# Kernel optimization log

Hardware: AMD Instinct MI355X
Metric: run time of the kernel (lower is better)

## Reference

```python
import jax, jax.numpy as jnp
import numpy as np

B, LQ, H, NH, LK, N = 32, 256, 256, 8, 512, 8192
DH = H // NH
EPS = 1e-12

def layer_norm(x, g, b):
    m = x.mean(-1, keepdims=True)
    v = ((x - m) ** 2).mean(-1, keepdims=True)
    return (x - m) / jnp.sqrt(v + EPS) * g + b

def setup_inputs() -> dict:
    rs = np.random.RandomState(0)
    counts = rs.randint(LK // 2, LK + 1, size=B)  # ragged per-graph edge counts, max = LK
    E = int(counts.sum())
    edge_batch = jnp.asarray(np.repeat(np.arange(B), counts), jnp.int32)
    edge_pos = jnp.asarray(np.concatenate([np.arange(c) for c in counts]), jnp.int32)
    pad_mask = jnp.asarray((np.arange(LK)[None, :] < counts[:, None]).astype(np.float32))
    src = jnp.asarray(rs.randint(0, N, E), jnp.int32)
    dst = jnp.asarray(rs.randint(0, N, E), jnp.int32)
    ks = jax.random.split(jax.random.key(0), 16)
    def rn(i, shape, s=0.02):
        return jax.random.normal(ks[i], shape, jnp.float32) * s
    return dict(
        extended_attention_mask=jnp.zeros((B, 1, 1, LQ), jnp.float32),
        query=rn(0, (B, LQ, H), 1.0),
        rel_embedding_output=rn(1, (E, H), 1.0),
        graph_output=rn(2, (N, H), 1.0),
        src=src, dst=dst, edge_batch=edge_batch, edge_pos=edge_pos, pad_mask=pad_mask,
        Wq=rn(3, (H, H)), bq=jnp.zeros((H,), jnp.float32),
        Wk=rn(4, (2 * H, H)), bk=jnp.zeros((H,), jnp.float32),
        Wv=rn(5, (H, H)), bv=jnp.zeros((H,), jnp.float32),
        Wo=rn(6, (H, H)), bo=jnp.zeros((H,), jnp.float32),
        ln1_g=jnp.ones((H,), jnp.float32), ln1_b=jnp.zeros((H,), jnp.float32),
        W1=rn(7, (H, H)), b1=jnp.zeros((H,), jnp.float32),
        W2=rn(8, (H, H)), b2=jnp.zeros((H,), jnp.float32),
        ln2_g=jnp.ones((H,), jnp.float32), ln2_b=jnp.zeros((H,), jnp.float32),
    )

def reference(extended_attention_mask, query, rel_embedding_output, graph_output,
              src, dst, edge_batch, edge_pos, pad_mask,
              Wq, bq, Wk, bk, Wv, bv, Wo, bo, ln1_g, ln1_b,
              W1, b1, W2, b2, ln2_g, ln2_b):
    # --- memory_transform: edge gather + ragged pad (vectorized scatter) ---
    key_flat = jnp.concatenate([graph_output[src], rel_embedding_output], -1)  # [E, 2H]
    dst_flat = graph_output[dst]                                               # [E, H]
    key_pad = jnp.zeros((B, LK, 2 * H), key_flat.dtype).at[edge_batch, edge_pos].set(key_flat)
    val_pad = jnp.zeros((B, LK, H), dst_flat.dtype).at[edge_batch, edge_pos].set(dst_flat)
    cross_mask = (1.0 - pad_mask)[:, None, None, :] * -10000.0                 # [B,1,1,LK]
    # --- BidiAttention ---
    Q = (query @ Wq + bq).reshape(B, LQ, NH, DH)
    K = (key_pad @ Wk + bk).reshape(B, LK, NH, DH)
    V = (val_pad @ Wv + bv).reshape(B, LK, NH, DH)
    scores = jnp.einsum('bqhd,bkhd->bhqk', Q, K) / np.float32(np.sqrt(DH))
    pq = jax.nn.softmax(scores + cross_mask, axis=-1)
    query_ctx = jnp.einsum('bhqk,bkhd->bqhd', pq, V).reshape(B, LQ, H)
    pv = jax.nn.softmax(scores.transpose(0, 1, 3, 2) + extended_attention_mask, axis=-1)
    value_ctx = jnp.einsum('bhkq,bqhd->bkhd', pv, Q).reshape(B, LK, H)
    # --- RelAwareCross output / gate ---
    query_out = layer_norm(query_ctx @ Wo + bo + query, ln1_g, ln1_b)
    theta = jax.nn.sigmoid(value_ctx @ W1 + b1 + val_pad @ W2 + b2)
    value_new = layer_norm(theta * value_ctx + (1.0 - theta) * val_pad, ln2_g, ln2_b)
    # --- memory_update: unpad + scatter-mean by dst, replace rows with incoming edges ---
    val_edges = value_new[edge_batch, edge_pos]                                # [E, H]
    sums = jax.ops.segment_sum(val_edges, dst, num_segments=N)
    cnts = jax.ops.segment_sum(jnp.ones((val_edges.shape[0],), val_edges.dtype), dst, num_segments=N)
    mean = sums / jnp.maximum(cnts, 1.0)[:, None]
    graph_new = jnp.where((cnts > 0)[:, None], mean, graph_output)
    return (graph_new, query_out)
```

## Files before the change

kernel.cpp:

```cpp
#include <hip/hip_runtime.h>
#include <hip/hip_bf16.h>
#include <string.h>

#define B_ 32
#define LQ_ 256
#define H_ 256
#define NH_ 8
#define LK_ 512
#define N_ 8192
#define DH_ 32

typedef float floatx4 __attribute__((ext_vector_type(4)));
typedef short shortx8 __attribute__((ext_vector_type(8)));
typedef short shortx4 __attribute__((ext_vector_type(4)));

__device__ __forceinline__ short f2b(float f) {
    __hip_bfloat16 h = __float2bfloat16(f);
    short s;
    __builtin_memcpy(&s, &h, 2);
    return s;
}
__device__ __forceinline__ float b2f(short s) {
    unsigned u = ((unsigned)(unsigned short)s) << 16;
    float f;
    __builtin_memcpy(&f, &u, 4);
    return f;
}

#define LOG2E 1.44269504088896f

__global__ __launch_bounds__(256) void phase1(
    const float* __restrict__ graph, const float* __restrict__ rel,
    const int* __restrict__ src, const int* __restrict__ dst,
    const int* __restrict__ eb, const int* __restrict__ ep,
    const float* __restrict__ pad_mask,
    const float* __restrict__ Wq, const float* __restrict__ Wk,
    const float* __restrict__ Wv, const float* __restrict__ Wo,
    const float* __restrict__ W1, const float* __restrict__ W2,
    short* __restrict__ WT, short* __restrict__ key_pad,
    short* __restrict__ val_pad, int* __restrict__ head,
    int* __restrict__ row2e, int E) {
    const int bid = blockIdx.x, tid = threadIdx.x;
    if (bid < 8192) {
        int row = bid * 2 + (tid >> 7);
        int t = tid & 127;
        int b = row >> 9, p = row & 511;
        bool valid = pad_mask[row] > 0.5f;
        size_t krow = (size_t)row * 512;
        size_t vrow = (size_t)row * 256;
        int kc = t * 4, vc = t * 2;
        if (valid) {
            int lo = 0, hi = E;
            while (lo < hi) { int mid = (lo + hi) >> 1; if (eb[mid] < b) lo = mid + 1; else hi = mid; }
            int e = lo + p;
            int s = src[e], d = dst[e];
            const float* sp = (kc < 256) ? (graph + (size_t)s * 256 + kc)
                                         : (rel + (size_t)e * 256 + (kc - 256));
            float4 k4 = *(const float4*)sp;
            key_pad[krow + kc + 0] = f2b(k4.x);
            key_pad[krow + kc + 1] = f2b(k4.y);
            key_pad[krow + kc + 2] = f2b(k4.z);
            key_pad[krow + kc + 3] = f2b(k4.w);
            float2 v2 = *(const float2*)(graph + (size_t)d * 256 + vc);
            val_pad[vrow + vc + 0] = f2b(v2.x);
            val_pad[vrow + vc + 1] = f2b(v2.y);
        } else {
            *(long long*)&key_pad[krow + kc] = 0;
            *(int*)&val_pad[vrow + vc] = 0;
        }
    } else if (bid < 9984) {
        int i = (bid - 8192) * 256 + tid;
        const float* s;
        int K, loc;
        if (i < 65536) { s = Wq; K = 256; loc = i; }
        else if (i < 196608) { s = Wk; K = 512; loc = i - 65536; }
        else {
            int m = (i - 196608) >> 16;
            loc = (i - 196608) & 65535;
            K = 256;
            s = (m == 0) ? Wv : (m == 1) ? Wo : (m == 2) ? W1 : W2;
        }
        int n = loc / K, k = loc - n * K;
        WT[i] = f2b(s[(size_t)k * 256 + n]);
    } else {
        int i = (bid - 9984) * 256 + tid;
        if (i < 8192) head[i] = -1;
        for (int j = i; j < E; j += 8192)
            row2e[eb[j] * 512 + ep[j]] = j;
    }
}

__global__ __launch_bounds__(256) void phase2_gemm(
    const float* __restrict__ query, const short* __restrict__ key_pad,
    const short* __restrict__ val_pad, const short* __restrict__ WT,
    const float* __restrict__ bq, const float* __restrict__ bk,
    const float* __restrict__ bv,
    short* __restrict__ Qb, short* __restrict__ Kb,
    short* __restrict__ Vt, short* __restrict__ Qt) {
    __shared__ short As[64][40];
    __shared__ short Bs[64][40];
    const int tid = threadIdx.x;
    const int id = blockIdx.x;
    const float* Af = nullptr; const short* Ab = nullptr;
    const float* Bf = nullptr; const short* Bb = nullptr;
    const float* bias; short* C;
    size_t cbase; int cstride, K; bool biasM;
    if (id < 512) {
        int rb = id >> 2, cb = id & 3;
        Af = query + (size_t)(rb * 64) * 256; K = 256;
        Bb = WT + (size_t)(cb * 64) * 256;
        bias = bq + cb * 64; biasM = false;
        C = Qb; cbase = (size_t)(rb * 64) * 256 + cb * 64; cstride = 256;
    } else if (id < 1536) {
        int t = id - 512; int rb = t >> 2, cb = t & 3;
        Ab = key_pad + (size_t)(rb * 64) * 512; K = 512;
        Bb = WT + 65536 + (size_t)(cb * 64) * 512;
        bias = bk + cb * 64; biasM = false;
        C = Kb; cbase = (size_t)(rb * 64) * 256 + cb * 64; cstride = 256;
    } else if (id < 2560) {
        int t = id - 1536; int b = t >> 5, ct = (t >> 3) & 3, kt = t & 7;
        Ab = WT + 196608 + (size_t)(ct * 64) * 256; K = 256;
        Bb = val_pad + ((size_t)(b * 512 + kt * 64)) * 256;
        bias = bv + ct * 64; biasM = true;
        C = Vt; cbase = ((size_t)(b * 256 + ct * 64)) * 512 + kt * 64; cstride = 512;
    } else {
        int t = id - 2560; int b = t >> 4, ct = (t >> 2) & 3, qt = t & 3;
        Ab = WT + (size_t)(ct * 64) * 256; K = 256;
        Bf = query + ((size_t)(b * 256 + qt * 64)) * 256;
        bias = bq + ct * 64; biasM = true;
        C = Qt; cbase = ((size_t)(b * 256 + ct * 64)) * 256 + qt * 64; cstride = 256;
    }
    const int wv = tid >> 6, lane = tid & 63;
    const int mw = (wv & 1) * 32, nw = (wv >> 1) * 32;
    const int lm = lane & 15, quad = lane >> 4;

    floatx4 acc[2][2] = {{{0.f, 0.f, 0.f, 0.f}, {0.f, 0.f, 0.f, 0.f}},
                         {{0.f, 0.f, 0.f, 0.f}, {0.f, 0.f, 0.f, 0.f}}};

    for (int kc = 0; kc < K; kc += 32) {
        int r = tid >> 2, kq = (tid & 3) * 8;
        if (Af) {
            const float* ap = Af + (size_t)r * K + kc + kq;
            float4 a1 = *(const float4*)ap, a2 = *(const float4*)(ap + 4);
            As[r][kq + 0] = f2b(a1.x); As[r][kq + 1] = f2b(a1.y);
            As[r][kq + 2] = f2b(a1.z); As[r][kq + 3] = f2b(a1.w);
            As[r][kq + 4] = f2b(a2.x); As[r][kq + 5] = f2b(a2.y);
            As[r][kq + 6] = f2b(a2.z); As[r][kq + 7] = f2b(a2.w);
        } else {
            *(shortx8*)&As[r][kq] = *(const shortx8*)(Ab + (size_t)r * K + kc + kq);
        }
        if (Bf) {
            const float* bp = Bf + (size_t)r * K + kc + kq;
            float4 b1 = *(const float4*)bp, b2 = *(const float4*)(bp + 4);
            Bs[r][kq + 0] = f2b(b1.x); Bs[r][kq + 1] = f2b(b1.y);
            Bs[r][kq + 2] = f2b(b1.z); Bs[r][kq + 3] = f2b(b1.w);
            Bs[r][kq + 4] = f2b(b2.x); Bs[r][kq + 5] = f2b(b2.y);
            Bs[r][kq + 6] = f2b(b2.z); Bs[r][kq + 7] = f2b(b2.w);
        } else {
            *(shortx8*)&Bs[r][kq] = *(const shortx8*)(Bb + (size_t)r * K + kc + kq);
        }
        __syncthreads();
        shortx8 a0 = *(const shortx8*)&As[mw + lm][quad * 8];
        shortx8 a1 = *(const shortx8*)&As[mw + 16 + lm][quad * 8];
        shortx8 b0 = *(const shortx8*)&Bs[nw + lm][quad * 8];
        shortx8 b1 = *(const shortx8*)&Bs[nw + 16 + lm][quad * 8];
        acc[0][0] = __builtin_amdgcn_mfma_f32_16x16x32_bf16(a0, b0, acc[0][0], 0, 0, 0);
        acc[0][1] = __builtin_amdgcn_mfma_f32_16x16x32_bf16(a0, b1, acc[0][1], 0, 0, 0);
        acc[1][0] = __builtin_amdgcn_mfma_f32_16x16x32_bf16(a1, b0, acc[1][0], 0, 0, 0);
        acc[1][1] = __builtin_amdgcn_mfma_f32_16x16x32_bf16(a1, b1, acc[1][1], 0, 0, 0);
        __syncthreads();
    }
#pragma unroll
    for (int i = 0; i < 2; i++) {
#pragma unroll
        for (int j = 0; j < 2; j++) {
            int gn = nw + j * 16 + lm;
#pragma unroll
            for (int r = 0; r < 4; r++) {
                int gm = mw + i * 16 + quad * 4 + r;
                float bvv = biasM ? bias[gm] : bias[gn];
                C[cbase + (size_t)gm * cstride + gn] = f2b(acc[i][j][r] + bvv);
            }
        }
    }
}

__global__ __launch_bounds__(512, 4) void phase3_attn(
    const short* __restrict__ Qm, const short* __restrict__ Km,
    const short* __restrict__ Vt, const short* __restrict__ Qt,
    const float* __restrict__ pad_mask, const float* __restrict__ ext,
    short* __restrict__ qctx, short* __restrict__ vctx) {
    __shared__ short SA[128][40];
    __shared__ short ST[32][136];
    __shared__ short P[8][32][72];
    const int tid = threadIdx.x;
    const int w = tid >> 6, lane = tid & 63;
    const int lm = lane & 15, quad = lane >> 4;
    const float scale2 = 0.17677669529663687f * LOG2E;
    const int id = blockIdx.x;
    short (*Pw)[72] = P[w];

    if (id < 256) {
        const int b = id >> 3, h = id & 7;
        shortx8 bqf[2];
        bqf[0] = *(const shortx8*)(Qm + ((size_t)(b * 256 + w * 32 + lm)) * 256 + h * 32 + quad * 8);
        bqf[1] = *(const shortx8*)(Qm + ((size_t)(b * 256 + w * 32 + 16 + lm)) * 256 + h * 32 + quad * 8);
        floatx4 oacc[2][2] = {{{0.f,0.f,0.f,0.f},{0.f,0.f,0.f,0.f}},
                              {{0.f,0.f,0.f,0.f},{0.f,0.f,0.f,0.f}}};
        float psum[2] = {0.f, 0.f};
        const floatx4* pmp = (const floatx4*)(pad_mask + b * 512);
        for (int kc = 0; kc < 512; kc += 128) {
            if (tid < 256) {
                int r = tid >> 1, dq = (tid & 1) * 16;
                const short* kp = Km + ((size_t)(b * 512 + kc + r)) * 256 + h * 32 + dq;
                *(shortx8*)&SA[r][dq] = *(const shortx8*)kp;
                *(shortx8*)&SA[r][dq + 8] = *(const shortx8*)(kp + 8);
            } else {
                int u = tid - 256;
                int r = u >> 3, kq = (u & 7) * 16;
                const short* vp = Vt + ((size_t)(b * 256 + h * 32 + r)) * 512 + kc + kq;
                *(shortx8*)&ST[r][kq] = *(const shortx8*)vp;
                *(shortx8*)&ST[r][kq + 8] = *(const shortx8*)(vp + 8);
            }
            __syncthreads();
#pragma unroll
            for (int kh = 0; kh < 2; kh++) {
#pragma unroll
                for (int kt = 0; kt < 4; kt++) {
                    shortx8 ak = *(const shortx8*)&SA[kh * 64 + kt * 16 + lm][quad * 8];
                    floatx4 pm = pmp[kc / 4 + kh * 16 + kt * 4 + quad];
#pragma unroll
                    for (int qf = 0; qf < 2; qf++) {
                        floatx4 s = {0.f, 0.f, 0.f, 0.f};
                        s = __builtin_amdgcn_mfma_f32_16x16x32_bf16(ak, bqf[qf], s, 0, 0, 0);
                        shortx4 p4;
#pragma unroll
                        for (int r = 0; r < 4; r++) {
                            float e = __builtin_amdgcn_exp2f(
                                s[r] * scale2 + (1.0f - pm[r]) * (-10000.0f * LOG2E));
                            psum[qf] += e;
                            p4[r] = f2b(e);
                        }
                        *(long long*)&Pw[qf * 16 + lm][kt * 16 + quad * 4] = *(long long*)&p4;
                    }
                }
#pragma unroll
                for (int ks = 0; ks < 2; ks++) {
#pragma unroll
                    for (int qf = 0; qf < 2; qf++) {
                        shortx8 pb = *(const shortx8*)&Pw[qf * 16 + lm][ks * 32 + quad * 8];
#pragma unroll
                        for (int di = 0; di < 2; di++) {
                            shortx8 av = *(const shortx8*)&ST[di * 16 + lm][kh * 64 + ks * 32 + quad * 8];
                            oacc[qf][di] = __builtin_amdgcn_mfma_f32_16x16x32_bf16(av, pb, oacc[qf][di], 0, 0, 0);
                        }
                    }
                }
            }
            __syncthreads();
        }
#pragma unroll
        for (int qf = 0; qf < 2; qf++) {
            psum[qf] += __shfl_xor(psum[qf], 16, 64);
            psum[qf] += __shfl_xor(psum[qf], 32, 64);
            float inv = 1.0f / psum[qf];
            int q = w * 32 + qf * 16 + lm;
            short* op = qctx + ((size_t)(b * 256 + q)) * 256 + h * 32;
#pragma unroll
            for (int di = 0; di < 2; di++) {
                shortx4 o;
#pragma unroll
                for (int r = 0; r < 4; r++) o[r] = f2b(oacc[qf][di][r] * inv);
                *(long long*)(op + di * 16 + quad * 4) = *(long long*)&o;
            }
        }
    } else {
        const int t = id - 256;
        const int b = t >> 4, h = (t >> 1) & 7, khb = t & 1;
        shortx8 bkf[2];
        bkf[0] = *(const shortx8*)(Km + ((size_t)(b * 512 + khb * 256 + w * 32 + lm)) * 256 + h * 32 + quad * 8);
        bkf[1] = *(const shortx8*)(Km + ((size_t)(b * 512 + khb * 256 + w * 32 + 16 + lm)) * 256 + h * 32 + quad * 8);
        floatx4 oacc[2][2] = {{{0.f,0.f,0.f,0.f},{0.f,0.f,0.f,0.f}},
                              {{0.f,0.f,0.f,0.f},{0.f,0.f,0.f,0.f}}};
        float psum[2] = {0.f, 0.f};
        const floatx4* emp = (const floatx4*)(ext + b * 256);
        for (int qc = 0; qc < 256; qc += 128) {
            if (tid < 256) {
                int r = tid >> 1, dq = (tid & 1) * 16;
                const short* qp = Qm + ((size_t)(b * 256 + qc + r)) * 256 + h * 32 + dq;
                *(shortx8*)&SA[r][dq] = *(const shortx8*)qp;
                *(shortx8*)&SA[r][dq + 8] = *(const shortx8*)(qp + 8);
            } else {
                int u = tid - 256;
                int r = u >> 3, kq = (u & 7) * 16;
                const short* tp = Qt + ((size_t)(b * 256 + h * 32 + r)) * 256 + qc + kq;
                *(shortx8*)&ST[r][kq] = *(const shortx8*)tp;
                *(shortx8*)&ST[r][kq + 8] = *(const shortx8*)(tp + 8);
            }
            __syncthreads();
#pragma unroll
            for (int qh = 0; qh < 2; qh++) {
#pragma unroll
                for (int qt = 0; qt < 4; qt++) {
                    shortx8 aq = *(const shortx8*)&SA[qh * 64 + qt * 16 + lm][quad * 8];
                    floatx4 em = emp[qc / 4 + qh * 16 + qt * 4 + quad];
#pragma unroll
                    for (int kf = 0; kf < 2; kf++) {
                        floatx4 s = {0.f, 0.f, 0.f, 0.f};
                        s = __builtin_amdgcn_mfma_f32_16x16x32_bf16(aq, bkf[kf], s, 0, 0, 0);
                        shortx4 p4;
#pragma unroll
                        for (int r = 0; r < 4; r++) {
                            float e = __builtin_amdgcn_exp2f(s[r] * scale2 + em[r] * LOG2E);
                            psum[kf] += e;
                            p4[r] = f2b(e);
                        }
                        *(long long*)&Pw[kf * 16 + lm][qt * 16 + quad * 4] = *(long long*)&p4;
                    }
                }
#pragma unroll
                for (int ks = 0; ks < 2; ks++) {
#pragma unroll
                    for (int kf = 0; kf < 2; kf++) {
                        shortx8 pb = *(const shortx8*)&Pw[kf * 16 + lm][ks * 32 + quad * 8];
#pragma unroll
                        for (int di = 0; di < 2; di++) {
                            shortx8 aT = *(const shortx8*)&ST[di * 16 + lm][qh * 64 + ks * 32 + quad * 8];
                            oacc[kf][di] = __builtin_amdgcn_mfma_f32_16x16x32_bf16(aT, pb, oacc[kf][di], 0, 0, 0);
                        }
                    }
                }
            }
            __syncthreads();
        }
#pragma unroll
        for (int kf = 0; kf < 2; kf++) {
            psum[kf] += __shfl_xor(psum[kf], 16, 64);
            psum[kf] += __shfl_xor(psum[kf], 32, 64);
            float inv = 1.0f / psum[kf];
            int k = khb * 256 + w * 32 + kf * 16 + lm;
            short* op = vctx + ((size_t)(b * 512 + k)) * 256 + h * 32;
#pragma unroll
            for (int di = 0; di < 2; di++) {
                shortx4 o;
#pragma unroll
                for (int r = 0; r < 4; r++) o[r] = f2b(oacc[kf][di][r] * inv);
                *(long long*)(op + di * 16 + quad * 4) = *(long long*)&o;
            }
        }
    }
}

__global__ __launch_bounds__(256) void phase4a_gemm(
    const short* __restrict__ qctx, const short* __restrict__ vctx,
    const short* __restrict__ val_pad, const short* __restrict__ WTo,
    const short* __restrict__ WT1, const short* __restrict__ WT2,
    float* __restrict__ obuf, float* __restrict__ tbuf) {
    __shared__ short As1[64][40];
    __shared__ short As2[64][40];
    __shared__ short Bs1[64][40];
    __shared__ short Bs2[64][40];
    const int tid = threadIdx.x;
    const int id = blockIdx.x;
    const bool is_out = id < 512;
    int t = is_out ? id : id - 512;
    const int row0 = (t >> 2) * 64, col0 = (t & 3) * 64;
    const int wv = tid >> 6, lane = tid & 63;
    const int mw = (wv & 1) * 32, nw = (wv >> 1) * 32;
    const int lm = lane & 15, quad = lane >> 4;

    floatx4 acc[2][2] = {{{0.f, 0.f, 0.f, 0.f}, {0.f, 0.f, 0.f, 0.f}},
                         {{0.f, 0.f, 0.f, 0.f}, {0.f, 0.f, 0.f, 0.f}}};

    for (int kc = 0; kc < 256; kc += 32) {
        int r = tid >> 2, kq = (tid & 3) * 8;
        if (is_out) {
            *(shortx8*)&As1[r][kq] =
                *(const shortx8*)(qctx + (size_t)(row0 + r) * 256 + kc + kq);
            *(shortx8*)&Bs1[r][kq] =
                *(const shortx8*)(WTo + (size_t)(col0 + r) * 256 + kc + kq);
        } else {
            *(shortx8*)&As1[r][kq] =
                *(const shortx8*)(vctx + (size_t)(row0 + r) * 256 + kc + kq);
            *(shortx8*)&As2[r][kq] =
                *(const shortx8*)(val_pad + (size_t)(row0 + r) * 256 + kc + kq);
            *(shortx8*)&Bs1[r][kq] =
                *(const shortx8*)(WT1 + (size_t)(col0 + r) * 256 + kc + kq);
            *(shortx8*)&Bs2[r][kq] =
                *(const shortx8*)(WT2 + (size_t)(col0 + r) * 256 + kc + kq);
        }
        __syncthreads();
        shortx8 a0 = *(const shortx8*)&As1[mw + lm][quad * 8];
        shortx8 a1 = *(const shortx8*)&As1[mw + 16 + lm][quad * 8];
        shortx8 b0 = *(const shortx8*)&Bs1[nw + lm][quad * 8];
        shortx8 b1 = *(const shortx8*)&Bs1[nw + 16 + lm][quad * 8];
        acc[0][0] = __builtin_amdgcn_mfma_f32_16x16x32_bf16(a0, b0, acc[0][0], 0, 0, 0);
        acc[0][1] = __builtin_amdgcn_mfma_f32_16x16x32_bf16(a0, b1, acc[0][1], 0, 0, 0);
        acc[1][0] = __builtin_amdgcn_mfma_f32_16x16x32_bf16(a1, b0, acc[1][0], 0, 0, 0);
        acc[1][1] = __builtin_amdgcn_mfma_f32_16x16x32_bf16(a1, b1, acc[1][1], 0, 0, 0);
        if (!is_out) {
            shortx8 c0 = *(const shortx8*)&As2[mw + lm][quad * 8];
            shortx8 c1 = *(const shortx8*)&As2[mw + 16 + lm][quad * 8];
            shortx8 d0 = *(const shortx8*)&Bs2[nw + lm][quad * 8];
            shortx8 d1 = *(const shortx8*)&Bs2[nw + 16 + lm][quad * 8];
            acc[0][0] = __builtin_amdgcn_mfma_f32_16x16x32_bf16(c0, d0, acc[0][0], 0, 0, 0);
            acc[0][1] = __builtin_amdgcn_mfma_f32_16x16x32_bf16(c0, d1, acc[0][1], 0, 0, 0);
            acc[1][0] = __builtin_amdgcn_mfma_f32_16x16x32_bf16(c1, d0, acc[1][0], 0, 0, 0);
            acc[1][1] = __builtin_amdgcn_mfma_f32_16x16x32_bf16(c1, d1, acc[1][1], 0, 0, 0);
        }
        __syncthreads();
    }
    float* C = is_out ? obuf : tbuf;
#pragma unroll
    for (int i = 0; i < 2; i++) {
#pragma unroll
        for (int j = 0; j < 2; j++) {
            int gn = col0 + nw + j * 16 + lm;
#pragma unroll
            for (int r = 0; r < 4; r++) {
                int gm = row0 + mw + i * 16 + quad * 4 + r;
                C[(size_t)gm * 256 + gn] = acc[i][j][r];
            }
        }
    }
}

__global__ __launch_bounds__(256) void phase4b_ln(
    const float* __restrict__ obuf, const float* __restrict__ bo,
    const float* __restrict__ query, const float* __restrict__ g1,
    const float* __restrict__ be1, float* __restrict__ out_q,
    float* __restrict__ tbuf, const short* __restrict__ vctx,
    const short* __restrict__ val_pad, const float* __restrict__ b1_,
    const float* __restrict__ b2_, const float* __restrict__ g2,
    const float* __restrict__ be2, const float* __restrict__ pad_mask,
    const int* __restrict__ row2e, const int* __restrict__ dst,
    int* __restrict__ head, int* __restrict__ nxt) {
    const int lane = threadIdx.x & 63, w = threadIdx.x >> 6;
    const int c0 = lane * 4;
    if (blockIdx.x < 2048) {
        int row = blockIdx.x * 4 + w;
        long long base = (long long)row * H_ + c0;
        float4 o = *(const float4*)(obuf + base);
        float4 bo4 = *(const float4*)(bo + c0);
        float4 q4 = *(const float4*)(query + base);
        float x0 = o.x + bo4.x + q4.x, x1 = o.y + bo4.y + q4.y;
        float x2 = o.z + bo4.z + q4.z, x3 = o.w + bo4.w + q4.w;
        float t = x0 + x1 + x2 + x3;
        for (int off = 32; off > 0; off >>= 1) t += __shfl_xor(t, off, 64);
        float mean = t * (1.0f / H_);
        float d0 = x0 - mean, d1 = x1 - mean, d2 = x2 - mean, d3 = x3 - mean;
        float v = d0 * d0 + d1 * d1 + d2 * d2 + d3 * d3;
        for (int off = 32; off > 0; off >>= 1) v += __shfl_xor(v, off, 64);
        float rs = rsqrtf(v * (1.0f / H_) + 1e-12f);
        float4 g = *(const float4*)(g1 + c0);
        float4 be = *(const float4*)(be1 + c0);
        float4 out;
        out.x = d0 * rs * g.x + be.x; out.y = d1 * rs * g.y + be.y;
        out.z = d2 * rs * g.z + be.z; out.w = d3 * rs * g.w + be.w;
        *(float4*)(out_q + base) = out;
    } else {
        int row = (blockIdx.x - 2048) * 4 + w;
        if (pad_mask[row] > 0.5f) {
            long long base = (long long)row * H_ + c0;
            float4 tb = *(const float4*)(tbuf + base);
            float4 b14 = *(const float4*)(b1_ + c0);
            float4 b24 = *(const float4*)(b2_ + c0);
            shortx4 vc = *(const shortx4*)(vctx + base);
            shortx4 vp = *(const shortx4*)(val_pad + base);
            float x[4];
#pragma unroll
            for (int j = 0; j < 4; j++) {
                float tv = (j == 0) ? tb.x : (j == 1) ? tb.y : (j == 2) ? tb.z : tb.w;
                float bb1 = (j == 0) ? b14.x : (j == 1) ? b14.y : (j == 2) ? b14.z : b14.w;
                float bb2 = (j == 0) ? b24.x : (j == 1) ? b24.y : (j == 2) ? b24.z : b24.w;
                float th = 1.0f / (1.0f + __expf(-(tv + bb1 + bb2)));
                x[j] = th * b2f(vc[j]) + (1.0f - th) * b2f(vp[j]);
            }
            float t = x[0] + x[1] + x[2] + x[3];
            for (int off = 32; off > 0; off >>= 1) t += __shfl_xor(t, off, 64);
            float mean = t * (1.0f / H_);
            float d0 = x[0] - mean, d1 = x[1] - mean, d2 = x[2] - mean, d3 = x[3] - mean;
            float v = d0 * d0 + d1 * d1 + d2 * d2 + d3 * d3;
            for (int off = 32; off > 0; off >>= 1) v += __shfl_xor(v, off, 64);
            float rs = rsqrtf(v * (1.0f / H_) + 1e-12f);
            float4 g = *(const float4*)(g2 + c0);
            float4 be = *(const float4*)(be2 + c0);
            float4 y4;
            y4.x = d0 * rs * g.x + be.x; y4.y = d1 * rs * g.y + be.y;
            y4.z = d2 * rs * g.z + be.z; y4.w = d3 * rs * g.w + be.w;
            *(float4*)(tbuf + base) = y4;
            if (lane == 0) {
                int d = dst[row2e[row]];
                int prev = atomicExch(&head[d], row);
                nxt[row] = prev;
            }
        }
    }
}

__global__ __launch_bounds__(256) void finalize_graph(
    const int* __restrict__ head, const int* __restrict__ nxt,
    const float* __restrict__ yrows, const float* __restrict__ graph,
    float* __restrict__ out_g) {
    int n = blockIdx.x, c = threadIdx.x;
    long long idx = (long long)n * H_ + c;
    int e = head[n];
    if (e < 0) { out_g[idx] = graph[idx]; return; }
    float acc = 0.f;
    int cnt = 0;
    while (e >= 0) {
        acc += yrows[(size_t)e * H_ + c];
        cnt++;
        e = nxt[e];
    }
    out_g[idx] = acc / (float)cnt;
}

extern "C" void kernel_launch(void* const* d_in, const int* in_sizes, int n_in,
                              void* d_out, int out_size, void* d_ws, size_t ws_size,
                              hipStream_t stream) {
    const float* ext_mask = (const float*)d_in[0];
    const float* query    = (const float*)d_in[1];
    const float* rel      = (const float*)d_in[2];
    const float* graph    = (const float*)d_in[3];
    const int*  src      = (const int*)d_in[4];
    const int*  dst      = (const int*)d_in[5];
    const int*  eb       = (const int*)d_in[6];
    const int*  ep       = (const int*)d_in[7];
    const float* pad_mask = (const float*)d_in[8];
    const float* Wq = (const float*)d_in[9];  const float* bq = (const float*)d_in[10];
    const float* Wk = (const float*)d_in[11]; const float* bk = (const float*)d_in[12];
    const float* Wv = (const float*)d_in[13]; const float* bv = (const float*)d_in[14];
    const float* Wo = (const float*)d_in[15]; const float* bo = (const float*)d_in[16];
    const float* g1 = (const float*)d_in[17]; const float* be1 = (const float*)d_in[18];
    const float* W1 = (const float*)d_in[19]; const float* b1 = (const float*)d_in[20];
    const float* W2 = (const float*)d_in[21]; const float* b2 = (const float*)d_in[22];
    const float* g2 = (const float*)d_in[23]; const float* be2 = (const float*)d_in[24];
    const int E = in_sizes[2] / H_;

    float* out_g = (float*)d_out;
    float* out_q = (float*)d_out + (size_t)N_ * H_;

    short* sp = (short*)d_ws;
    short* key_pad = sp; sp += (size_t)B_ * LK_ * 2 * H_;
    short* val_pad = sp; sp += (size_t)B_ * LK_ * H_;
    short* Qb      = sp; sp += (size_t)B_ * LQ_ * H_;
    short* Kb      = sp; sp += (size_t)B_ * LK_ * H_;
    short* Vt      = sp; sp += (size_t)B_ * H_ * LK_;
    short* Qt      = sp; sp += (size_t)B_ * H_ * LQ_;
    short* qctx    = sp; sp += (size_t)B_ * LQ_ * H_;
    short* vctx    = sp; sp += (size_t)B_ * LK_ * H_;
    short* WT      = sp; sp += 458752;
    short* WTo = WT + 262144;
    short* WT1 = WT + 327680;
    short* WT2 = WT + 393216;
    int* ip = (int*)(((size_t)sp + 15) & ~(size_t)15);
    int* head  = ip; ip += N_;
    int* nxt   = ip; ip += B_ * LK_;
    int* row2e = ip; ip += B_ * LK_;
    float* fp = (float*)ip;
    float* obuf = fp; fp += (size_t)B_ * LQ_ * H_;
    float* tbuf = fp; fp += (size_t)B_ * LK_ * H_;

    phase1<<<10016, 256, 0, stream>>>(graph, rel, src, dst, eb, ep, pad_mask,
                                      Wq, Wk, Wv, Wo, W1, W2,
                                      WT, key_pad, val_pad, head, row2e, E);
    phase2_gemm<<<3072, 256, 0, stream>>>(query, key_pad, val_pad, WT,
                                          bq, bk, bv, Qb, Kb, Vt, Qt);
    phase3_attn<<<768, 512, 0, stream>>>(Qb, Kb, Vt, Qt, pad_mask, ext_mask,
                                         qctx, vctx);
    phase4a_gemm<<<1536, 256, 0, stream>>>(qctx, vctx, val_pad, WTo, WT1, WT2,
                                           obuf, tbuf);
    phase4b_ln<<<6144, 256, 0, stream>>>(obuf, bo, query, g1, be1, out_q,
                                         tbuf, vctx, val_pad, b1, b2, g2, be2,
                                         pad_mask, row2e, dst, head, nxt);
    finalize_graph<<<N_, 256, 0, stream>>>(head, nxt, tbuf, graph, out_g);
}
```

Baseline: 245.1 us.

## Enlarge GEMM tiles to 128x128 per block with 4x4 MFMA per wave

Both projection GEMM kernels move from 64x64 output tiles, where each wave computes 2x2 MFMA fragments, to 128x128 tiles, where each wave computes 4x4 fragments. Each thread now stages 16 elements per K step instead of 8. The aim is more reuse of each shared-memory fragment and fewer global loads per output, at the cost of more accumulator registers. The grids shrink from 3072 to 768 blocks and from 1536 to 384 blocks, which may leave some compute units idle or lower occupancy. In phase4a the two operand pairs now run as sequential K passes through a single shared buffer.

Measured after the change: 237.5 us. 1.03x faster.

```diff
diff --git a/kernel.cpp b/kernel.cpp
--- a/kernel.cpp
+++ b/kernel.cpp
@@ -97,87 +97,107 @@
     const float* __restrict__ bv,
     short* __restrict__ Qb, short* __restrict__ Kb,
     short* __restrict__ Vt, short* __restrict__ Qt) {
-    __shared__ short As[64][40];
-    __shared__ short Bs[64][40];
+    __shared__ short As[128][40];
+    __shared__ short Bs[128][40];
     const int tid = threadIdx.x;
     const int id = blockIdx.x;
     const float* Af = nullptr; const short* Ab = nullptr;
     const float* Bf = nullptr; const short* Bb = nullptr;
     const float* bias; short* C;
     size_t cbase; int cstride, K; bool biasM;
-    if (id < 512) {
-        int rb = id >> 2, cb = id & 3;
-        Af = query + (size_t)(rb * 64) * 256; K = 256;
-        Bb = WT + (size_t)(cb * 64) * 256;
-        bias = bq + cb * 64; biasM = false;
-        C = Qb; cbase = (size_t)(rb * 64) * 256 + cb * 64; cstride = 256;
-    } else if (id < 1536) {
-        int t = id - 512; int rb = t >> 2, cb = t & 3;
-        Ab = key_pad + (size_t)(rb * 64) * 512; K = 512;
-        Bb = WT + 65536 + (size_t)(cb * 64) * 512;
-        bias = bk + cb * 64; biasM = false;
-        C = Kb; cbase = (size_t)(rb * 64) * 256 + cb * 64; cstride = 256;
-    } else if (id < 2560) {
-        int t = id - 1536; int b = t >> 5, ct = (t >> 3) & 3, kt = t & 7;
-        Ab = WT + 196608 + (size_t)(ct * 64) * 256; K = 256;
-        Bb = val_pad + ((size_t)(b * 512 + kt * 64)) * 256;
-        bias = bv + ct * 64; biasM = true;
-        C = Vt; cbase = ((size_t)(b * 256 + ct * 64)) * 512 + kt * 64; cstride = 512;
+    if (id < 128) {
+        int mt = id >> 1, nt = id & 1;
+        Af = query + (size_t)(mt * 128) * 256; K = 256;
+        Bb = WT + (size_t)(nt * 128) * 256;
+        bias = bq + nt * 128; biasM = false;
+        C = Qb; cbase = (size_t)(mt * 128) * 256 + nt * 128; cstride = 256;
+    } else if (id < 384) {
+        int t = id - 128; int mt = t >> 1, nt = t & 1;
+        Ab = key_pad + (size_t)(mt * 128) * 512; K = 512;
+        Bb = WT + 65536 + (size_t)(nt * 128) * 512;
+        bias = bk + nt * 128; biasM = false;
+        C = Kb; cbase = (size_t)(mt * 128) * 256 + nt * 128; cstride = 256;
+    } else if (id < 640) {
+        int t = id - 384; int b = t >> 3, ct = (t >> 2) & 1, nt = t & 3;
+        Ab = WT + 196608 + (size_t)(ct * 128) * 256; K = 256;
+        Bb = val_pad + ((size_t)(b * 512 + nt * 128)) * 256;
+        bias = bv + ct * 128; biasM = true;
+        C = Vt; cbase = ((size_t)(b * 256 + ct * 128)) * 512 + nt * 128; cstride = 512;
     } else {
-        int t = id - 2560; int b = t >> 4, ct = (t >> 2) & 3, qt = t & 3;
-        Ab = WT + (size_t)(ct * 64) * 256; K = 256;
-        Bf = query + ((size_t)(b * 256 + qt * 64)) * 256;
-        bias = bq + ct * 64; biasM = true;
-        C = Qt; cbase = ((size_t)(b * 256 + ct * 64)) * 256 + qt * 64; cstride = 256;
-    }
-    const int wv = tid >> 6, lane = tid & 63;
-    const int mw = (wv & 1) * 32, nw = (wv >> 1) * 32;
+        int t = id - 640; int b = t >> 2, ct = (t >> 1) & 1, qt = t & 1;
+        Ab = WT + (size_t)(ct * 128) * 256; K = 256;
+        Bf = query + ((size_t)(b * 256 + qt * 128)) * 256;
+        bias = bq + ct * 128; biasM = true;
+        C = Qt; cbase = ((size_t)(b * 256 + ct * 128)) * 256 + qt * 128; cstride = 256;
+    }
+    const int w = tid >> 6, lane = tid & 63;
+    const int R0 = (w >> 1) * 64, C0 = (w & 1) * 64;
     const int lm = lane & 15, quad = lane >> 4;
-
-    floatx4 acc[2][2] = {{{0.f, 0.f, 0.f, 0.f}, {0.f, 0.f, 0.f, 0.f}},
-                         {{0.f, 0.f, 0.f, 0.f}, {0.f, 0.f, 0.f, 0.f}}};
+    const int sr = tid >> 1, skq = (tid & 1) * 16;
+
+    floatx4 acc[4][4];
+#pragma unroll
+    for (int i = 0; i < 4; i++)
+#pragma unroll
+        for (int j = 0; j < 4; j++) acc[i][j] = {0.f, 0.f, 0.f, 0.f};
 
     for (int kc = 0; kc < K; kc += 32) {
-        int r = tid >> 2, kq = (tid & 3) * 8;
         if (Af) {
-            const float* ap = Af + (size_t)r * K + kc + kq;
+            const float* ap = Af + (size_t)sr * K + kc + skq;
             float4 a1 = *(const float4*)ap, a2 = *(const float4*)(ap + 4);
-            As[r][kq + 0] = f2b(a1.x); As[r][kq + 1] = f2b(a1.y);
-            As[r][kq + 2] = f2b(a1.z); As[r][kq + 3] = f2b(a1.w);
-            As[r][kq + 4] = f2b(a2.x); As[r][kq + 5] = f2b(a2.y);
-            As[r][kq + 6] = f2b(a2.z); As[r][kq + 7] = f2b(a2.w);
+            float4 a3 = *(const float4*)(ap + 8), a4 = *(const float4*)(ap + 12);
+            As[sr][skq + 0] = f2b(a1.x); As[sr][skq + 1] = f2b(a1.y);
+            As[sr][skq + 2] = f2b(a1.z); As[sr][skq + 3] = f2b(a1.w);
+            As[sr][skq + 4] = f2b(a2.x); As[sr][skq + 5] = f2b(a2.y);
+            As[sr][skq + 6] = f2b(a2.z); As[sr][skq + 7] = f2b(a2.w);
+            As[sr][skq + 8] = f2b(a3.x); As[sr][skq + 9] = f2b(a3.y);
+            As[sr][skq + 10] = f2b(a3.z); As[sr][skq + 11] = f2b(a3.w);
+            As[sr][skq + 12] = f2b(a4.x); As[sr][skq + 13] = f2b(a4.y);
+            As[sr][skq + 14] = f2b(a4.z); As[sr][skq + 15] = f2b(a4.w);
         } else {
-            *(shortx8*)&As[r][kq] = *(const shortx8*)(Ab + (size_t)r * K + kc + kq);
+            const short* ap = Ab + (size_t)sr * K + kc + skq;
+            *(shortx8*)&As[sr][skq] = *(const shortx8*)ap;
+            *(shortx8*)&As[sr][skq + 8] = *(const shortx8*)(ap + 8);
         }
         if (Bf) {
-            const float* bp = Bf + (size_t)r * K + kc + kq;
-            float4 b1 = *(const float4*)bp, b2 = *(const float4*)(bp + 4);
-            Bs[r][kq + 0] = f2b(b1.x); Bs[r][kq + 1] = f2b(b1.y);
-            Bs[r][kq + 2] = f2b(b1.z); Bs[r][kq + 3] = f2b(b1.w);
-            Bs[r][kq + 4] = f2b(b2.x); Bs[r][kq + 5] = f2b(b2.y);
-            Bs[r][kq + 6] = f2b(b2.z); Bs[r][kq + 7] = f2b(b2.w);
+            const float* bp = Bf + (size_t)sr * K + kc + skq;
+            float4 a1 = *(const float4*)bp, a2 = *(const float4*)(bp + 4);
+            float4 a3 = *(const float4*)(bp + 8), a4 = *(const float4*)(bp + 12);
+            Bs[sr][skq + 0] = f2b(a1.x); Bs[sr][skq + 1] = f2b(a1.y);
+            Bs[sr][skq + 2] = f2b(a1.z); Bs[sr][skq + 3] = f2b(a1.w);
+            Bs[sr][skq + 4] = f2b(a2.x); Bs[sr][skq + 5] = f2b(a2.y);
+            Bs[sr][skq + 6] = f2b(a2.z); Bs[sr][skq + 7] = f2b(a2.w);
+            Bs[sr][skq + 8] = f2b(a3.x); Bs[sr][skq + 9] = f2b(a3.y);
+            Bs[sr][skq + 10] = f2b(a3.z); Bs[sr][skq + 11] = f2b(a3.w);
+            Bs[sr][skq + 12] = f2b(a4.x); Bs[sr][skq + 13] = f2b(a4.y);
+            Bs[sr][skq + 14] = f2b(a4.z); Bs[sr][skq + 15] = f2b(a4.w);
         } else {
-            *(shortx8*)&Bs[r][kq] = *(const shortx8*)(Bb + (size_t)r * K + kc + kq);
+            const short* bp = Bb + (size_t)sr * K + kc + skq;
+            *(shortx8*)&Bs[sr][skq] = *(const shortx8*)bp;
+            *(shortx8*)&Bs[sr][skq + 8] = *(const shortx8*)(bp + 8);
         }
         __syncthreads();
-        shortx8 a0 = *(const shortx8*)&As[mw + lm][quad * 8];
-        shortx8 a1 = *(const shortx8*)&As[mw + 16 + lm][quad * 8];
-        shortx8 b0 = *(const shortx8*)&Bs[nw + lm][quad * 8];
-        shortx8 b1 = *(const shortx8*)&Bs[nw + 16 + lm][quad * 8];
-        acc[0][0] = __builtin_amdgcn_mfma_f32_16x16x32_bf16(a0, b0, acc[0][0], 0, 0, 0);
-        acc[0][1] = __builtin_amdgcn_mfma_f32_16x16x32_bf16(a0, b1, acc[0][1], 0, 0, 0);
-        acc[1][0] = __builtin_amdgcn_mfma_f32_16x16x32_bf16(a1, b0, acc[1][0], 0, 0, 0);
-        acc[1][1] = __builtin_amdgcn_mfma_f32_16x16x32_bf16(a1, b1, acc[1][1], 0, 0, 0);
+        shortx8 af[4], bf[4];
+#pragma unroll
+        for (int i = 0; i < 4; i++) {
+            af[i] = *(const shortx8*)&As[R0 + i * 16 + lm][quad * 8];
+            bf[i] = *(const shortx8*)&Bs[C0 + i * 16 + lm][quad * 8];
+        }
+#pragma unroll
+        for (int i = 0; i < 4; i++)
+#pragma unroll
+            for (int j = 0; j < 4; j++)
+                acc[i][j] = __builtin_amdgcn_mfma_f32_16x16x32_bf16(af[i], bf[j], acc[i][j], 0, 0, 0);
         __syncthreads();
     }
 #pragma unroll
-    for (int i = 0; i < 2; i++) {
-#pragma unroll
-        for (int j = 0; j < 2; j++) {
-            int gn = nw + j * 16 + lm;
+    for (int i = 0; i < 4; i++) {
+#pragma unroll
+        for (int j = 0; j < 4; j++) {
+            int gn = C0 + j * 16 + lm;
 #pragma unroll
             for (int r = 0; r < 4; r++) {
-                int gm = mw + i * 16 + quad * 4 + r;
+                int gm = R0 + i * 16 + quad * 4 + r;
                 float bvv = biasM ? bias[gm] : bias[gn];
                 C[cbase + (size_t)gm * cstride + gn] = f2b(acc[i][j][r] + bvv);
             }
@@ -356,70 +376,65 @@
     const short* __restrict__ val_pad, const short* __restrict__ WTo,
     const short* __restrict__ WT1, const short* __restrict__ WT2,
     float* __restrict__ obuf, float* __restrict__ tbuf) {
-    __shared__ short As1[64][40];
-    __shared__ short As2[64][40];
-    __shared__ short Bs1[64][40];
-    __shared__ short Bs2[64][40];
+    __shared__ short As[128][40];
+    __shared__ short Bs[128][40];
     const int tid = threadIdx.x;
     const int id = blockIdx.x;
-    const bool is_out = id < 512;
-    int t = is_out ? id : id - 512;
-    const int row0 = (t >> 2) * 64, col0 = (t & 3) * 64;
-    const int wv = tid >> 6, lane = tid & 63;
-    const int mw = (wv & 1) * 32, nw = (wv >> 1) * 32;
+    const bool is_out = id < 128;
+    int t = is_out ? id : id - 128;
+    const int mt = t >> 1, nt = t & 1;
+    const int w = tid >> 6, lane = tid & 63;
+    const int R0 = (w >> 1) * 64, C0 = (w & 1) * 64;
     const int lm = lane & 15, quad = lane >> 4;
-
-    floatx4 acc[2][2] = {{{0.f, 0.f, 0.f, 0.f}, {0.f, 0.f, 0.f, 0.f}},
-                         {{0.f, 0.f, 0.f, 0.f}, {0.f, 0.f, 0.f, 0.f}}};
-
-    for (int kc = 0; kc < 256; kc += 32) {
-        int r = tid >> 2, kq = (tid & 3) * 8;
-        if (is_out) {
-            *(shortx8*)&As1[r][kq] =
-                *(const shortx8*)(qctx + (size_t)(row0 + r) * 256 + kc + kq);
-            *(shortx8*)&Bs1[r][kq] =
-                *(const shortx8*)(WTo + (size_t)(col0 + r) * 256 + kc + kq);
-        } else {
-            *(shortx8*)&As1[r][kq] =
-                *(const shortx8*)(vctx + (size_t)(row0 + r) * 256 + kc + kq);
-            *(shortx8*)&As2[r][kq] =
-                *(const shortx8*)(val_pad + (size_t)(row0 + r) * 256 + kc + kq);
-            *(shortx8*)&Bs1[r][kq] =
-                *(const shortx8*)(WT1 + (size_t)(col0 + r) * 256 + kc + kq);
-            *(shortx8*)&Bs2[r][kq] =
-                *(const shortx8*)(WT2 + (size_t)(col0 + r) * 256 + kc + kq);
-        }
-        __syncthreads();
-        shortx8 a0 = *(const shortx8*)&As1[mw + lm][quad * 8];
-        shortx8 a1 = *(const shortx8*)&As1[mw + 16 + lm][quad * 8];
-        shortx8 b0 = *(const shortx8*)&Bs1[nw + lm][quad * 8];
-        shortx8 b1 = *(const shortx8*)&Bs1[nw + 16 + lm][quad * 8];
-        acc[0][0] = __builtin_amdgcn_mfma_f32_16x16x32_bf16(a0, b0, acc[0][0], 0, 0, 0);
-        acc[0][1] = __builtin_amdgcn_mfma_f32_16x16x32_bf16(a0, b1, acc[0][1], 0, 0, 0);
-        acc[1][0] = __builtin_amdgcn_mfma_f32_16x16x32_bf16(a1, b0, acc[1][0], 0, 0, 0);
-        acc[1][1] = __builtin_amdgcn_mfma_f32_16x16x32_bf16(a1, b1, acc[1][1], 0, 0, 0);
-        if (!is_out) {
-            shortx8 c0 = *(const shortx8*)&As2[mw + lm][quad * 8];
-            shortx8 c1 = *(const shortx8*)&As2[mw + 16 + lm][quad * 8];
-            shortx8 d0 = *(const shortx8*)&Bs2[nw + lm][quad * 8];
-            shortx8 d1 = *(const shortx8*)&Bs2[nw + 16 + lm][quad * 8];
-            acc[0][0] = __builtin_amdgcn_mfma_f32_16x16x32_bf16(c0, d0, acc[0][0], 0, 0, 0);
-            acc[0][1] = __builtin_amdgcn_mfma_f32_16x16x32_bf16(c0, d1, acc[0][1], 0, 0, 0);
-            acc[1][0] = __builtin_amdgcn_mfma_f32_16x16x32_bf16(c1, d0, acc[1][0], 0, 0, 0);
-            acc[1][1] = __builtin_amdgcn_mfma_f32_16x16x32_bf16(c1, d1, acc[1][1], 0, 0, 0);
-        }
-        __syncthreads();
+    const int sr = tid >> 1, skq = (tid & 1) * 16;
+    const int npair = is_out ? 1 : 2;
+
+    floatx4 acc[4][4];
+#pragma unroll
+    for (int i = 0; i < 4; i++)
+#pragma unroll
+        for (int j = 0; j < 4; j++) acc[i][j] = {0.f, 0.f, 0.f, 0.f};
+
+    for (int pair = 0; pair < npair; pair++) {
+        const short* Ap = is_out ? (qctx + (size_t)(mt * 128) * 256)
+                                 : (pair == 0 ? vctx + (size_t)(mt * 128) * 256
+                                              : val_pad + (size_t)(mt * 128) * 256);
+        const short* Bp = is_out ? (WTo + (size_t)(nt * 128) * 256)
+                                 : (pair == 0 ? WT1 + (size_t)(nt * 128) * 256
+                                              : WT2 + (size_t)(nt * 128) * 256);
+        for (int kc = 0; kc < 256; kc += 32) {
+            const short* ap = Ap + (size_t)sr * 256 + kc + skq;
+            *(shortx8*)&As[sr][skq] = *(const shortx8*)ap;
+            *(shortx8*)&As[sr][skq + 8] = *(const shortx8*)(ap + 8);
+            const short* bp = Bp + (size_t)sr * 256 + kc + skq;
+            *(shortx8*)&Bs[sr][skq] = *(const shortx8*)bp;
+            *(shortx8*)&Bs[sr][skq + 8] = *(const shortx8*)(bp + 8);
+            __syncthreads();
+            shortx8 af[4], bf[4];
+#pragma unroll
+            for (int i = 0; i < 4; i++) {
+                af[i] = *(const shortx8*)&As[R0 + i * 16 + lm][quad * 8];
+                bf[i] = *(const shortx8*)&Bs[C0 + i * 16 + lm][quad * 8];
+            }
+#pragma unroll
+            for (int i = 0; i < 4; i++)
+#pragma unroll
+                for (int j = 0; j < 4; j++)
+                    acc[i][j] = __builtin_amdgcn_mfma_f32_16x16x32_bf16(af[i], bf[j], acc[i][j], 0, 0, 0);
+            __syncthreads();
+        }
     }
     float* C = is_out ? obuf : tbuf;
-#pragma unroll
-    for (int i = 0; i < 2; i++) {
-#pragma unroll
-        for (int j = 0; j < 2; j++) {
-            int gn = col0 + nw + j * 16 + lm;
+    const size_t cbase = (size_t)(mt * 128) * 256 + nt * 128;
+#pragma unroll
+    for (int i = 0; i < 4; i++) {
+#pragma unroll
+        for (int j = 0; j < 4; j++) {
+            int gn = C0 + j * 16 + lm;
 #pragma unroll
             for (int r = 0; r < 4; r++) {
-                int gm = row0 + mw + i * 16 + quad * 4 + r;
-                C[(size_t)gm * 256 + gn] = acc[i][j][r];
+                int gm = R0 + i * 16 + quad * 4 + r;
+                C[cbase + (size_t)gm * 256 + gn] = acc[i][j][r];
             }
         }
     }
@@ -565,12 +580,12 @@
     phase1<<<10016, 256, 0, stream>>>(graph, rel, src, dst, eb, ep, pad_mask,
                                       Wq, Wk, Wv, Wo, W1, W2,
                                       WT, key_pad, val_pad, head, row2e, E);
-    phase2_gemm<<<3072, 256, 0, stream>>>(query, key_pad, val_pad, WT,
-                                          bq, bk, bv, Qb, Kb, Vt, Qt);
+    phase2_gemm<<<768, 256, 0, stream>>>(query, key_pad, val_pad, WT,
+                                         bq, bk, bv, Qb, Kb, Vt, Qt);
     phase3_attn<<<768, 512, 0, stream>>>(Qb, Kb, Vt, Qt, pad_mask, ext_mask,
                                          qctx, vctx);
-    phase4a_gemm<<<1536, 256, 0, stream>>>(qctx, vctx, val_pad, WTo, WT1, WT2,
-                                           obuf, tbuf);
+    phase4a_gemm<<<384, 256, 0, stream>>>(qctx, vctx, val_pad, WTo, WT1, WT2,
+                                          obuf, tbuf);
     phase4b_ln<<<6144, 256, 0, stream>>>(obuf, bo, query, g1, be1, out_q,
                                          tbuf, vctx, val_pad, b1, b2, g2, be2,
                                          pad_mask, row2e, dst, head, nxt);
```
